# Kernel optimization log

Hardware: AMD Instinct MI355X
Metric: run time of the kernel (lower is better)

The kernel has to match this reference:

```python
import jax, jax.numpy as jnp
import numpy as np
from jax import lax

K = 3
STRIDE = 1
PAD = 1


def setup_inputs() -> dict:
    key = jax.random.key(0)
    k1, k2, k3 = jax.random.split(key, 3)
    x = jax.random.normal(k1, (4, 256, 64, 64), dtype=jnp.float32)
    # offset-conv weight: C_in=256 -> 2*K*K=18 offset channels
    w_off = jax.random.normal(k2, (18, 256, 3, 3), dtype=jnp.float32) * 0.01
    # deformable conv weight: C_in=256 -> C_out=256
    w_def = jax.random.normal(k3, (256, 256, 3, 3), dtype=jnp.float32) * 0.05
    return {"x": x, "w_off": w_off, "w_def": w_def}


def _deform_conv(x, offset, w_def):
    # x: [B,C,H,W]; offset: [B,2*K*K,Ho,Wo] torchvision layout (dy,dx interleaved)
    B, C, H, W = x.shape
    Ho, Wo = offset.shape[2], offset.shape[3]
    KK = K * K
    off = offset.reshape(B, KK, 2, Ho, Wo)
    ky, kx = jnp.meshgrid(jnp.arange(K), jnp.arange(K), indexing="ij")
    ky = ky.reshape(KK).astype(x.dtype)  # kernel tap row offsets
    kx = kx.reshape(KK).astype(x.dtype)
    base_y = (jnp.arange(Ho, dtype=x.dtype) * STRIDE - PAD)[None, :, None] + ky[:, None, None]  # [KK,Ho,1]
    base_x = (jnp.arange(Wo, dtype=x.dtype) * STRIDE - PAD)[None, None, :] + kx[:, None, None]  # [KK,1,Wo]
    py = off[:, :, 0] + base_y  # [B,KK,Ho,Wo]
    px = off[:, :, 1] + base_x

    def sample_one(img, py1, px1):
        # img: [C,H,W]; py1/px1: [KK,Ho,Wo]
        y0f = jnp.floor(py1)
        x0f = jnp.floor(px1)
        wy1 = py1 - y0f
        wx1 = px1 - x0f
        wy0 = 1.0 - wy1
        wx0 = 1.0 - wx1
        y0 = y0f.astype(jnp.int32)
        x0 = x0f.astype(jnp.int32)
        y1 = y0 + 1
        x1 = x0 + 1

        def gather(yi, xi):
            valid = (yi >= 0) & (yi < H) & (xi >= 0) & (xi < W)
            yc = jnp.clip(yi, 0, H - 1)
            xc = jnp.clip(xi, 0, W - 1)
            v = img[:, yc, xc]  # [C,KK,Ho,Wo]
            return v * valid[None].astype(img.dtype)

        out = (wy0 * wx0)[None] * gather(y0, x0)
        out = out + (wy0 * wx1)[None] * gather(y0, x1)
        out = out + (wy1 * wx0)[None] * gather(y1, x0)
        out = out + (wy1 * wx1)[None] * gather(y1, x1)
        return out  # [C,KK,Ho,Wo]

    sampled = jax.vmap(sample_one)(x, py, px)  # [B,C,KK,Ho,Wo]
    w = w_def.reshape(w_def.shape[0], C, KK)
    return jnp.einsum("bckhw,ock->bohw", sampled, w)


def reference(x, w_off, w_def):
    offset = lax.conv_general_dilated(
        x, w_off, window_strides=(STRIDE, STRIDE),
        padding=[(PAD, PAD), (PAD, PAD)],
        dimension_numbers=("NCHW", "OIHW", "NCHW"),
    )
    return _deform_conv(x, offset, w_def)
```

## Files before the change

kernel.cpp:

```cpp
#include <hip/hip_runtime.h>

typedef __attribute__((ext_vector_type(8))) short short8;
typedef __attribute__((ext_vector_type(4))) float f32x4;
typedef __attribute__((ext_vector_type(4))) unsigned int u32x4;
typedef unsigned short ushort_t;

constexpr int B   = 4;
constexpr int C   = 256;
constexpr int H   = 64;
constexpr int W   = 64;
constexpr int HW  = H * W;
constexpr int OCH = 256;
constexpr int KT  = 9 * C;
constexpr int NHS = KT / 32;

__device__ __forceinline__ ushort_t f2bf(float f) {
    unsigned u = __float_as_uint(f);
    u += 0x7FFF + ((u >> 16) & 1);
    return (ushort_t)(u >> 16);
}

__device__ __forceinline__ void block_sync_lds() {
    asm volatile("s_waitcnt lgkmcnt(0)" ::: "memory");
    __builtin_amdgcn_s_barrier();
    asm volatile("" ::: "memory");
}

__global__ __launch_bounds__(256) void prep_all(
    const float* __restrict__ x, const float* __restrict__ w_def,
    const float* __restrict__ w_off, ushort_t* __restrict__ xt01,
    ushort_t* __restrict__ xtD, ushort_t* __restrict__ wPack,
    ushort_t* __restrict__ wOffA)
{
    __shared__ float sT[64][65];
    int blk = blockIdx.x;
    if (blk < 1024) {
        int cg  = blk & 3;
        int y   = (blk >> 2) & 63;
        int b   = blk >> 8;
        int t   = threadIdx.x;
        int col = t & 63, r4 = t >> 6;

        const float* xp = x + (((size_t)b * C + cg * 64) * H + y) * W;
        #pragma unroll
        for (int i = 0; i < 16; ++i) {
            int cl = i * 4 + r4;
            sT[cl][col] = xp[(size_t)cl * HW + col];
        }
        __syncthreads();
        ushort_t* base = (b < 2) ? (xt01 + (size_t)b * HW * C)
                                 : (xtD + (size_t)(b - 2) * HW * C);
        ushort_t* op = base + ((size_t)y * W) * C + cg * 64;
        #pragma unroll
        for (int i = 0; i < 16; ++i) {
            int xl = i * 4 + r4;
            op[(size_t)xl * C + col] = f2bf(sT[col][xl]);
        }
    } else {
        int tid = (blk - 1024) * 256 + threadIdx.x;
        if (tid < NHS * 16 * 64) {
            int lane = tid & 63;
            int o = ((tid >> 6) & 15) * 16 + (lane & 15);
            int kbase = (tid >> 10) * 32 + (lane >> 4) * 8;
            union { ushort_t u[8]; short8 v; } pk;
            #pragma unroll
            for (int j = 0; j < 8; ++j) {
                int kidx = kbase + j;
                int c = kidx & 255, tap = kidx >> 8;
                pk.u[j] = f2bf(w_def[((size_t)o * C + c) * 9 + tap]);
            }
            *(short8*)(wPack + (size_t)tid * 8) = pk.v;
        } else {
            int t2 = tid - NHS * 16 * 64;
            int lane = t2 & 63;
            int o = ((t2 >> 6) & 1) * 16 + (lane & 15);
            int kbase = (t2 >> 7) * 32 + (lane >> 4) * 8;
            union { ushort_t u[8]; short8 v; } pk;
            #pragma unroll
            for (int j = 0; j < 8; ++j) {
                int kidx = kbase + j;
                int c = kidx & 255, tap = kidx >> 8;
                pk.u[j] = (o < 18) ? f2bf(w_off[((size_t)o * C + c) * 9 + tap]) : (ushort_t)0;
            }
            *(short8*)(wOffA + (size_t)t2 * 8) = pk.v;
        }
    }
}

__global__ __launch_bounds__(512, 2) void deform_pair(
    const ushort_t* __restrict__ xtB, const ushort_t* __restrict__ wOffA,
    const ushort_t* __restrict__ wPack, float* __restrict__ out, int pbase)
{
    __shared__ __align__(16) ushort_t sS[2][16][33][8];
    __shared__ float sOff[18][32];
    __shared__ float sPart[8][18][32];
    __shared__ int   sBase[2][128];
    __shared__ float sWgt[2][32][4];

    int orig = blockIdx.x;
    int r = ((orig & 7) << 5) | (orig >> 3);
    int bl = r >> 7, ho = (r >> 1) & 63, pxh = r & 1;
    int tid = threadIdx.x;
    int lane = tid & 63, wv = tid >> 6;
    int chunk = tid & 15, rq = (tid >> 4) & 31;

    const ushort_t* xtb = xtB + (size_t)bl * HW * C;
    int b = pbase + bl;

    {
        const short8* wA = (const short8*)wOffA;
        f32x4 pacc[2][2];
        #pragma unroll
        for (int i = 0; i < 2; ++i)
            #pragma unroll
            for (int j = 0; j < 2; ++j) pacc[i][j] = (f32x4){0.f, 0.f, 0.f, 0.f};

        #pragma unroll 1
        for (int i = 0; i < 9; ++i) {
            int ks = wv * 9 + i;
            int tap = ks >> 3, cs = ks & 7;
            int ky = tap / 3, kx = tap - ky * 3;
            int y  = ho - 1 + ky;
            int yc = min(max(y, 0), 63);
            bool yok = ((unsigned)y < 64u);
            short8 a0 = wA[(size_t)ks * 128 + lane];
            short8 a1 = wA[(size_t)ks * 128 + 64 + lane];
            #pragma unroll
            for (int pt = 0; pt < 2; ++pt) {
                int px = pxh * 32 + pt * 16 + (lane & 15);
                int xx = px - 1 + kx;
                bool ok = yok && ((unsigned)xx < 64u);
                unsigned msk = ok ? 0xffffffffu : 0u;
                int xc = min(max(xx, 0), 63);
                const ushort_t* srcb = xtb + (size_t)(yc * 64 + xc) * C
                                       + cs * 32 + (lane >> 4) * 8;
                union { u32x4 u; short8 s; } bv;
                bv.u = *(const u32x4*)srcb;
                bv.u[0] &= msk; bv.u[1] &= msk; bv.u[2] &= msk; bv.u[3] &= msk;
                pacc[0][pt] = __builtin_amdgcn_mfma_f32_16x16x32_bf16(a0, bv.s, pacc[0][pt], 0, 0, 0);
                pacc[1][pt] = __builtin_amdgcn_mfma_f32_16x16x32_bf16(a1, bv.s, pacc[1][pt], 0, 0, 0);
            }
        }
        #pragma unroll
        for (int gt = 0; gt < 2; ++gt) {
            #pragma unroll
            for (int pt = 0; pt < 2; ++pt) {
                #pragma unroll
                for (int j = 0; j < 4; ++j) {
                    int oc = gt * 16 + (lane >> 4) * 4 + j;
                    if (oc < 18)
                        sPart[wv][oc][pt * 16 + (lane & 15)] = pacc[gt][pt][j];
                }
            }
        }
    }
    __syncthreads();
    for (int idx = tid; idx < 18 * 32; idx += 512) {
        int oc = idx >> 5, q = idx & 31;
        float s = 0.f;
        #pragma unroll
        for (int g = 0; g < 8; ++g) s += sPart[g][oc][q];
        sOff[oc][q] = s;
    }
    __syncthreads();

    f32x4 acc2[2][2];
    #pragma unroll
    for (int i = 0; i < 2; ++i)
        #pragma unroll
        for (int j = 0; j < 2; ++j) acc2[i][j] = (f32x4){0.f, 0.f, 0.f, 0.f};

    auto computeBase = [&](int tap, int buf) {
        if (tid < 128) {
            int n = tid >> 5, q = tid & 31;
            int ky = tap / 3, kx = tap - ky * 3;
            float offy = sOff[2 * tap][q];
            float offx = sOff[2 * tap + 1][q];
            float py  = offy + (float)(ho - 1 + ky);
            float pxf = offx + (float)(pxh * 32 + q - 1 + kx);
            float y0f = floorf(py), x0f = floorf(pxf);
            float wy1 = py - y0f, wx1 = pxf - x0f;
            int y0 = (int)y0f, x0 = (int)x0f;
            int dy = n >> 1, dx = n & 1;
            int yy = y0 + dy, xx = x0 + dx;
            float wn = (dy ? wy1 : (1.f - wy1)) * (dx ? wx1 : (1.f - wx1));
            wn *= (((unsigned)yy < 64u) ? 1.f : 0.f) * (((unsigned)xx < 64u) ? 1.f : 0.f);
            int yc = min(max(yy, 0), 63), xc = min(max(xx, 0), 63);
            sBase[buf][tid] = (yc * 64 + xc) * C;
            sWgt[buf][q][n] = wn;
        }
    };

    auto loadBases = [&](int buf, int* rb) {
        #pragma unroll
        for (int n = 0; n < 4; ++n) rb[n] = sBase[buf][n * 32 + rq];
    };

    auto issueC = [&](const int* rb, int sub, u32x4* L) {
        #pragma unroll
        for (int n = 0; n < 4; ++n)
            L[n] = *(const u32x4*)(xtb + rb[n] + sub * 128 + chunk * 8);
    };

    auto blendDirect = [&](const u32x4* L, const float* w, int p) {
        unsigned pk[4];
        #pragma unroll
        for (int j = 0; j < 4; ++j) {
            float f0l = __uint_as_float(L[0][j] << 16);
            float f0h = __uint_as_float(L[0][j] & 0xffff0000u);
            float f1l = __uint_as_float(L[1][j] << 16);
            float f1h = __uint_as_float(L[1][j] & 0xffff0000u);
            float f2l = __uint_as_float(L[2][j] << 16);
            float f2h = __uint_as_float(L[2][j] & 0xffff0000u);
            float f3l = __uint_as_float(L[3][j] << 16);
            float f3h = __uint_as_float(L[3][j] & 0xffff0000u);
            float lo = fmaf(w[0], f0l, fmaf(w[1], f1l, fmaf(w[2], f2l, w[3] * f3l)));
            float hi = fmaf(w[0], f0h, fmaf(w[1], f1h, fmaf(w[2], f2h, w[3] * f3h)));
            asm("v_cvt_pk_bf16_f32 %0, %1, %2" : "=v"(pk[j]) : "v"(lo), "v"(hi));
        }
        u32x4 wvec = (u32x4){pk[0], pk[1], pk[2], pk[3]};
        *(u32x4*)&sS[p][chunk][rq][0] = wvec;
    };

    int gt0 = wv * 2;
    const short8* wpB = (const short8*)wPack;

    auto loadA8 = [&](int ks4base, short8* A) {
        #pragma unroll
        for (int h = 0; h < 4; ++h) {
            size_t an = ((size_t)(ks4base + h) * 16 + gt0) * 64 + lane;
            A[2 * h]     = wpB[an];
            A[2 * h + 1] = wpB[an + 64];
        }
    };

    auto mfmaPhase = [&](const short8* A, int p) {
        __builtin_amdgcn_s_setprio(1);
        #pragma unroll
        for (int h = 0; h < 4; ++h) {
            #pragma unroll
            for (int pt = 0; pt < 2; ++pt) {
                short8 bF = *(const short8*)&sS[p][h * 4 + (lane >> 4)][pt * 16 + (lane & 15)][0];
                acc2[0][pt] = __builtin_amdgcn_mfma_f32_16x16x32_bf16(A[2 * h],     bF, acc2[0][pt], 0, 0, 0);
                acc2[1][pt] = __builtin_amdgcn_mfma_f32_16x16x32_bf16(A[2 * h + 1], bF, acc2[1][pt], 0, 0, 0);
            }
        }
        __builtin_amdgcn_s_setprio(0);
    };

    u32x4 LA[4], LB[4];
    short8 A[8];

    computeBase(0, 0);
    block_sync_lds();
    {
        int rb0[4];
        loadBases(0, rb0);
        issueC(rb0, 0, LA);
        issueC(rb0, 1, LB);
    }

    int p = 0;
    #pragma unroll 1
    for (int tap = 0; tap < 9; ++tap) {
        float wcur[4];
        *(float4*)&wcur[0] = *(const float4*)&sWgt[tap & 1][rq][0];
        if (tap < 8) computeBase(tap + 1, (tap + 1) & 1);

        int rb[4];
        loadA8(tap * 8, A);
        blendDirect(LA, wcur, p);
        block_sync_lds();
        if (tap < 8) { loadBases((tap + 1) & 1, rb); issueC(rb, 0, LA); }
        mfmaPhase(A, p);
        p ^= 1;
        loadA8(tap * 8 + 4, A);
        blendDirect(LB, wcur, p);
        block_sync_lds();
        if (tap < 8) issueC(rb, 1, LB);
        mfmaPhase(A, p);
        p ^= 1;
    }

    #pragma unroll
    for (int ot = 0; ot < 2; ++ot) {
        int o = wv * 32 + ot * 16 + (lane >> 4) * 4;
        #pragma unroll
        for (int pt = 0; pt < 2; ++pt) {
            int pxx = pxh * 32 + pt * 16 + (lane & 15);
            #pragma unroll
            for (int j = 0; j < 4; ++j)
                out[(((size_t)b * OCH + (o + j)) * H + ho) * W + pxx] = acc2[ot][pt][j];
        }
    }
}

extern "C" void kernel_launch(void* const* d_in, const int* in_sizes, int n_in,
                              void* d_out, int out_size, void* d_ws, size_t ws_size,
                              hipStream_t stream)
{
    const float* x     = (const float*)d_in[0];
    const float* w_off = (const float*)d_in[1];
    const float* w_def = (const float*)d_in[2];
    float* out = (float*)d_out;

    ushort_t* xt01  = (ushort_t*)d_ws;
    ushort_t* wPack = xt01 + (size_t)2 * HW * C;
    ushort_t* wOffA = wPack + (size_t)NHS * 16 * 64 * 8;
    ushort_t* xtD   = (ushort_t*)d_out;

    prep_all<<<1348, 256, 0, stream>>>(x, w_def, w_off, xt01, xtD, wPack, wOffA);
    deform_pair<<<256, 512, 0, stream>>>(xtD, wOffA, wPack, out, 2);
    deform_pair<<<256, 512, 0, stream>>>(xt01, wOffA, wPack, out, 0);
}
```

Measured before the change: 66.46 us.

## Merge per-tap half-phases into one blend and barrier per tap

Each tap now blends both channel halves into a doubled shared-memory staging buffer and uses a single barrier before running both MFMA halves, instead of two blend/barrier/MFMA sub-phases. Gathers for both halves of the next tap are issued together right after that barrier. The aim is fewer block barriers and longer runs of latency hiding for the gathers. In exchange, LDS use per block doubles, which may limit occupancy at 2 blocks per CU.

```diff
diff --git a/kernel.cpp b/kernel.cpp
--- a/kernel.cpp
+++ b/kernel.cpp
@@ -91,7 +91,7 @@
     const ushort_t* __restrict__ xtB, const ushort_t* __restrict__ wOffA,
     const ushort_t* __restrict__ wPack, float* __restrict__ out, int pbase)
 {
-    __shared__ __align__(16) ushort_t sS[2][16][33][8];
+    __shared__ __align__(16) ushort_t sS[2][32][33][8];
     __shared__ float sOff[18][32];
     __shared__ float sPart[8][18][32];
     __shared__ int   sBase[2][128];
@@ -196,13 +196,16 @@
         for (int n = 0; n < 4; ++n) rb[n] = sBase[buf][n * 32 + rq];
     };
 
-    auto issueC = [&](const int* rb, int sub, u32x4* L) {
-        #pragma unroll
-        for (int n = 0; n < 4; ++n)
-            L[n] = *(const u32x4*)(xtb + rb[n] + sub * 128 + chunk * 8);
-    };
-
-    auto blendDirect = [&](const u32x4* L, const float* w, int p) {
+    auto issueBoth = [&](const int* rb, u32x4* La, u32x4* Lb) {
+        #pragma unroll
+        for (int n = 0; n < 4; ++n) {
+            const ushort_t* p0 = xtb + rb[n] + chunk * 8;
+            La[n] = *(const u32x4*)p0;
+            Lb[n] = *(const u32x4*)(p0 + 128);
+        }
+    };
+
+    auto blendOne = [&](const u32x4* L, const float* w, int p, int slot) {
         unsigned pk[4];
         #pragma unroll
         for (int j = 0; j < 4; ++j) {
@@ -219,7 +222,7 @@
             asm("v_cvt_pk_bf16_f32 %0, %1, %2" : "=v"(pk[j]) : "v"(lo), "v"(hi));
         }
         u32x4 wvec = (u32x4){pk[0], pk[1], pk[2], pk[3]};
-        *(u32x4*)&sS[p][chunk][rq][0] = wvec;
+        *(u32x4*)&sS[p][slot][rq][0] = wvec;
     };
 
     int gt0 = wv * 2;
@@ -234,13 +237,13 @@
         }
     };
 
-    auto mfmaPhase = [&](const short8* A, int p) {
+    auto mfmaHalf = [&](const short8* A, int p, int half) {
         __builtin_amdgcn_s_setprio(1);
         #pragma unroll
         for (int h = 0; h < 4; ++h) {
             #pragma unroll
             for (int pt = 0; pt < 2; ++pt) {
-                short8 bF = *(const short8*)&sS[p][h * 4 + (lane >> 4)][pt * 16 + (lane & 15)][0];
+                short8 bF = *(const short8*)&sS[p][half * 16 + h * 4 + (lane >> 4)][pt * 16 + (lane & 15)][0];
                 acc2[0][pt] = __builtin_amdgcn_mfma_f32_16x16x32_bf16(A[2 * h],     bF, acc2[0][pt], 0, 0, 0);
                 acc2[1][pt] = __builtin_amdgcn_mfma_f32_16x16x32_bf16(A[2 * h + 1], bF, acc2[1][pt], 0, 0, 0);
             }
@@ -256,8 +259,7 @@
     {
         int rb0[4];
         loadBases(0, rb0);
-        issueC(rb0, 0, LA);
-        issueC(rb0, 1, LB);
+        issueBoth(rb0, LA, LB);
     }
 
     int p = 0;
@@ -267,18 +269,17 @@
         *(float4*)&wcur[0] = *(const float4*)&sWgt[tap & 1][rq][0];
         if (tap < 8) computeBase(tap + 1, (tap + 1) & 1);
 
+        loadA8(tap * 8, A);
+        blendOne(LA, wcur, p, chunk);
+        blendOne(LB, wcur, p, 16 + chunk);
+        block_sync_lds();
+
         int rb[4];
-        loadA8(tap * 8, A);
-        blendDirect(LA, wcur, p);
-        block_sync_lds();
-        if (tap < 8) { loadBases((tap + 1) & 1, rb); issueC(rb, 0, LA); }
-        mfmaPhase(A, p);
-        p ^= 1;
+        if (tap < 8) { loadBases((tap + 1) & 1, rb); issueBoth(rb, LA, LB); }
+
+        mfmaHalf(A, p, 0);
         loadA8(tap * 8 + 4, A);
-        blendDirect(LB, wcur, p);
-        block_sync_lds();
-        if (tap < 8) issueC(rb, 1, LB);
-        mfmaPhase(A, p);
+        mfmaHalf(A, p, 1);
         p ^= 1;
     }
 
```

Result: faster. 64.78 us (median of 2 runs) (-2.5%).
